# Kernel tuning notes

Hardware: AMD Instinct MI355X
Metric: run time of the kernel (lower is better)

## Reference

```python
import jax, jax.numpy as jnp
import numpy as np

N = 50000      # nodes
E = 800000     # edges (before self-loops)
D_IN = 64
D_OUT = 64


def setup_inputs() -> dict:
    key = jax.random.key(0)
    k1, k2, k3 = jax.random.split(key, 3)
    x = jax.random.normal(k1, (N, D_IN), dtype=jnp.float32)
    edge_index = jax.random.randint(k2, (2, E), 0, N, dtype=jnp.int64)
    # Glorot-ish init for the GCN linear weight
    W = jax.random.normal(k3, (D_IN, D_OUT), dtype=jnp.float32) * (1.0 / np.sqrt(D_IN))
    b = jnp.zeros((D_OUT,), dtype=jnp.float32)
    return {"x": x, "edge_index": edge_index, "W": W, "b": b}


def reference(x, edge_index, W, b):
    # GCNConv: add self-loops, symmetric normalization D^-1/2 (A+I) D^-1/2,
    # linear transform, scatter-add aggregation, bias; then ReLU.
    # Dropout is treated in eval mode (identity) for determinism.
    n = x.shape[0]
    loop = jnp.arange(n, dtype=edge_index.dtype)
    src = jnp.concatenate([edge_index[0], loop])  # [E+N]
    dst = jnp.concatenate([edge_index[1], loop])  # [E+N]

    ones = jnp.ones(src.shape[0], dtype=x.dtype)
    deg = jax.ops.segment_sum(ones, dst, num_segments=n)            # [N]
    dis = jnp.where(deg > 0, jax.lax.rsqrt(deg), 0.0)               # deg^-1/2
    norm = dis[src] * dis[dst]                                      # [E+N]

    xw = x @ W                                                      # [N, D_OUT]
    msgs = norm[:, None] * xw[src]                                  # [E+N, D_OUT]
    out = jax.ops.segment_sum(msgs, dst, num_segments=n) + b        # [N, D_OUT]
    return jax.nn.relu(out)
```

## Files before the change

### kernel.cpp

```cpp
#include <hip/hip_runtime.h>


#define TPB 256
#define STPB 512
#define MAXDEG 64
#define OVFCAP 8192
#define EPB 4096
#define MAXBIN 1024
#define MAXBLK 256

__device__ __forceinline__ int edges_are_i32(const unsigned* __restrict__ w) {
    int lane = threadIdx.x & 63;
    unsigned v = w[1 + 2 * lane];
    return __ballot(v != 0u) != 0ull;
}

__device__ __forceinline__ unsigned short f2bf(float f) {
    unsigned u = __float_as_uint(f);
    u += 0x7FFFu + ((u >> 16) & 1u);
    return (unsigned short)(u >> 16);
}
__device__ __forceinline__ float bf2f(unsigned short h) {
    return __uint_as_float(((unsigned)h) << 16);
}
__device__ __forceinline__ unsigned scale2(unsigned v, float dd) {
    unsigned lo = (unsigned)f2bf(dd * bf2f((unsigned short)(v & 0xFFFFu)));
    unsigned hi = (unsigned)f2bf(dd * bf2f((unsigned short)(v >> 16)));
    return lo | (hi << 16);
}

__device__ __forceinline__ void load4(const void* ei, int is32, long long base, int* v) {
    if (is32) {
        int4 a = *(const int4*)((const int*)ei + base);
        v[0] = a.x; v[1] = a.y; v[2] = a.z; v[3] = a.w;
    } else {
        longlong4 a = *(const longlong4*)((const long long*)ei + base);
        v[0] = (int)a.x; v[1] = (int)a.y; v[2] = (int)a.z; v[3] = (int)a.w;
    }
}

__global__ __launch_bounds__(256) void gemm_z0(const float* __restrict__ x,
                                               const float* __restrict__ W,
                                               unsigned short* __restrict__ z0,
                                               unsigned* __restrict__ ovf, int n) {
    if (blockIdx.x == 0 && threadIdx.x == 0) *ovf = 0u;

    __shared__ float lw[4096];
    const int t = threadIdx.x;
#pragma unroll
    for (int i = 0; i < 16; ++i) lw[i * 256 + t] = W[i * 256 + t];
    __syncthreads();

    const int lane = t & 63;
    const int wv   = t >> 6;
    const int row0 = blockIdx.x * 32 + wv * 8;
    if (row0 >= n) return;
    const int nr = (n - row0 >= 8) ? 8 : (n - row0);

    float acc[8] = {0.f, 0.f, 0.f, 0.f, 0.f, 0.f, 0.f, 0.f};
#pragma unroll
    for (int k0 = 0; k0 < 16; ++k0) {
        const float w0 = lw[(4 * k0 + 0) * 64 + lane];
        const float w1 = lw[(4 * k0 + 1) * 64 + lane];
        const float w2 = lw[(4 * k0 + 2) * 64 + lane];
        const float w3 = lw[(4 * k0 + 3) * 64 + lane];
#pragma unroll
        for (int r = 0; r < 8; ++r) {
            if (r < nr) {
                float4 xv = *(const float4*)(x + (long long)(row0 + r) * 64 + 4 * k0);
                acc[r] = fmaf(xv.w, w3, fmaf(xv.z, w2, fmaf(xv.y, w1,
                         fmaf(xv.x, w0, acc[r]))));
            }
        }
    }
#pragma unroll
    for (int r = 0; r < 8; ++r)
        if (r < nr) z0[(long long)(row0 + r) * 64 + lane] = f2bf(acc[r]);
}

__global__ __launch_bounds__(512) void binsort(const void* __restrict__ ei,
                                               unsigned* __restrict__ arena,
                                               uint2* __restrict__ desc,
                                               int E, int nbins, int nblocks) {
    __shared__ unsigned hist[MAXBIN];
    __shared__ unsigned bstart[MAXBIN];
    __shared__ unsigned cur[MAXBIN];
    __shared__ unsigned sorted[EPB];
    __shared__ unsigned partial[STPB];
    const int t   = threadIdx.x;
    const int blk = blockIdx.x;
    const long long base = (long long)blk * EPB;
    const int cnt = (int)((E - base < EPB) ? (E - base) : EPB);
    const int is32 = edges_are_i32((const unsigned*)ei);

    for (int i = t; i < nbins; i += STPB) hist[i] = 0u;
    __syncthreads();

    unsigned pay[8];
    unsigned short bn[8];
#pragma unroll
    for (int r = 0; r < 2; ++r) {
        const int lo = r * (STPB * 4) + t * 4;
        if (lo + 4 <= cnt) {
            int s4[4], d4[4];
            load4(ei, is32, base + lo, s4);
            load4(ei, is32, (long long)E + base + lo, d4);
#pragma unroll
            for (int k = 0; k < 4; ++k) {
                pay[r * 4 + k] = ((unsigned)(d4[k] & 63) << 16) | (unsigned)s4[k];
                bn[r * 4 + k]  = (unsigned short)((unsigned)d4[k] >> 6);
                atomicAdd(&hist[bn[r * 4 + k]], 1u);
            }
        } else {
#pragma unroll
            for (int k = 0; k < 4; ++k) {
                int l = lo + k;
                if (l < cnt) {
                    int s_, d_;
                    if (is32) {
                        s_ = ((const int*)ei)[base + l];
                        d_ = ((const int*)ei)[(long long)E + base + l];
                    } else {
                        s_ = (int)((const long long*)ei)[base + l];
                        d_ = (int)((const long long*)ei)[(long long)E + base + l];
                    }
                    pay[r * 4 + k] = ((unsigned)(d_ & 63) << 16) | (unsigned)s_;
                    bn[r * 4 + k]  = (unsigned short)((unsigned)d_ >> 6);
                    atomicAdd(&hist[bn[r * 4 + k]], 1u);
                } else {
                    bn[r * 4 + k] = 0xFFFFu;
                }
            }
        }
    }
    __syncthreads();

    unsigned s0 = 0;
#pragma unroll
    for (int k = 0; k < 2; ++k) { int bq = t * 2 + k; if (bq < nbins) s0 += hist[bq]; }
    partial[t] = s0;
    __syncthreads();
    for (int o = 1; o < STPB; o <<= 1) {
        unsigned v = (t >= o) ? partial[t - o] : 0u;
        __syncthreads();
        partial[t] += v;
        __syncthreads();
    }
    unsigned run = (t == 0) ? 0u : partial[t - 1];
#pragma unroll
    for (int k = 0; k < 2; ++k) {
        int bq = t * 2 + k;
        if (bq < nbins) { bstart[bq] = run; cur[bq] = run; run += hist[bq]; }
    }
    __syncthreads();

#pragma unroll
    for (int i = 0; i < 8; ++i) {
        if (bn[i] != 0xFFFFu) {
            unsigned p = atomicAdd(&cur[bn[i]], 1u);
            sorted[p] = pay[i];
        }
    }
    __syncthreads();

    for (int i = t; i < cnt; i += STPB) arena[base + i] = sorted[i];
    for (int bq = t; bq < nbins; bq += STPB) {
        uint2 dd;
        dd.x = (unsigned)(base + bstart[bq]);
        dd.y = hist[bq];
        desc[(long long)blk * nbins + bq] = dd;
    }
}

__global__ __launch_bounds__(256) void build_ell(const uint2* __restrict__ desc,
                                                 const unsigned* __restrict__ arena,
                                                 unsigned* __restrict__ fc,
                                                 unsigned short* __restrict__ ell,
                                                 unsigned* __restrict__ ovf,
                                                 int* __restrict__ ovfList,
                                                 unsigned short* __restrict__ z,
                                                 int n, int nbins, int nblocks) {
    __shared__ unsigned segstart[MAXBLK];
    __shared__ unsigned segpre[MAXBLK];
    __shared__ unsigned pre[256];
    __shared__ unsigned lcnt[MAXDEG];
    __shared__ __align__(16) unsigned short lell[MAXDEG * MAXDEG];
    const int t   = threadIdx.x;
    const int bin = blockIdx.x;
    const int base = bin * MAXDEG;

    if (t < MAXDEG) lcnt[t] = 0u;

    unsigned len = 0;
    if (t < nblocks) {
        uint2 dd = desc[(long long)t * nbins + bin];
        segstart[t] = dd.x;
        len = dd.y;
    }
    pre[t] = len;
    __syncthreads();
    for (int o = 1; o < 256; o <<= 1) {
        unsigned v = (t >= o) ? pre[t - o] : 0u;
        __syncthreads();
        pre[t] += v;
        __syncthreads();
    }
    const unsigned total = pre[255];
    if (t < nblocks) segpre[t] = pre[t] - len;
    __syncthreads();

    for (unsigned j = t; j < total; j += 256) {
        int lo = 0, hi = nblocks - 1;
        while (lo < hi) {
            int mid = (lo + hi + 1) >> 1;
            if (segpre[mid] <= j) lo = mid; else hi = mid - 1;
        }
        unsigned e  = arena[segstart[lo] + (j - segpre[lo])];
        unsigned dl = e >> 16;
        unsigned c  = atomicAdd(&lcnt[dl], 1u);
        if (c < MAXDEG) {
            lell[dl * MAXDEG + c] = (unsigned short)(e & 0xFFFFu);
        } else {
            unsigned p = atomicAdd(ovf, 1u);
            if (p < OVFCAP) {
                ovfList[2 * p]     = (int)(e & 0xFFFFu);
                ovfList[2 * p + 1] = base + (int)dl;
            }
        }
    }
    __syncthreads();

    const int maxrow = (n - base < MAXDEG) ? (n - base) : MAXDEG;
    if (t < maxrow) fc[base + t] = lcnt[t];

    const uint4* lp = (const uint4*)lell;
    uint4* gp = (uint4*)(ell + (long long)base * MAXDEG);
    for (int i = t; i < maxrow * 8; i += 256) gp[i] = lp[i];

    uint4* zp = (uint4*)(z + (long long)base * 64);
    for (int i = t; i < maxrow * 8; i += 256) {
        int row = i >> 3;
        float dd = rsqrtf(1.0f + (float)lcnt[row]);
        uint4 v = zp[i];
        v.x = scale2(v.x, dd); v.y = scale2(v.y, dd);
        v.z = scale2(v.z, dd); v.w = scale2(v.w, dd);
        zp[i] = v;
    }
}

__global__ __launch_bounds__(256) void gather_z(const unsigned short* __restrict__ ell,
                                                const unsigned* __restrict__ fc,
                                                const unsigned* __restrict__ ovf,
                                                const int* __restrict__ ovfList,
                                                const unsigned short* __restrict__ z,
                                                const float* __restrict__ b,
                                                float* __restrict__ out, int n) {
    const int wv   = (int)threadIdx.x >> 6;
    const int lane = threadIdx.x & 63;
    const int half = lane >> 5;
    const int cp   = lane & 31;
    const int node = (blockIdx.x * 4 + wv) * 2 + half;
    const bool valid = node < n;
    const int nodec = valid ? node : (n - 1);

    const unsigned deg = valid ? fc[nodec] : 0u;
    const float dd = rsqrtf(1.0f + (float)deg);

    unsigned zs = *(const unsigned*)(z + (unsigned)nodec * 64 + cp * 2);
    float acc0 = bf2f((unsigned short)(zs & 0xFFFFu));
    float acc1 = bf2f((unsigned short)(zs >> 16));

    unsigned m = deg < MAXDEG ? deg : MAXDEG;
    if (!valid) m = 0u;
    const unsigned mo = __shfl_xor((int)m, 32);
    const unsigned mmax = m > mo ? m : mo;

    const uint4* prow = (const uint4*)(ell + (unsigned)nodec * MAXDEG);

    unsigned i = 0;
    for (; i + 8 <= mmax; i += 8) {
        uint4 rw = prow[i >> 3];
        unsigned s[8];
        s[0] = rw.x & 0xFFFFu; s[1] = rw.x >> 16;
        s[2] = rw.y & 0xFFFFu; s[3] = rw.y >> 16;
        s[4] = rw.z & 0xFFFFu; s[5] = rw.z >> 16;
        s[6] = rw.w & 0xFFFFu; s[7] = rw.w >> 16;
        if (i + 8 <= m) {
            unsigned v[8];
#pragma unroll
            for (int k = 0; k < 8; ++k)
                v[k] = *(const unsigned*)(z + s[k] * 64u + cp * 2);
#pragma unroll
            for (int k = 0; k < 8; ++k) {
                acc0 += bf2f((unsigned short)(v[k] & 0xFFFFu));
                acc1 += bf2f((unsigned short)(v[k] >> 16));
            }
        } else {
#pragma unroll
            for (int k = 0; k < 8; ++k) {
                if (i + k < m) {
                    unsigned v = *(const unsigned*)(z + s[k] * 64u + cp * 2);
                    acc0 += bf2f((unsigned short)(v & 0xFFFFu));
                    acc1 += bf2f((unsigned short)(v >> 16));
                }
            }
        }
    }
    for (; i < mmax; ++i) {
        if (i < m) {
            unsigned s = ell[(unsigned)nodec * MAXDEG + i];
            unsigned v = *(const unsigned*)(z + s * 64u + cp * 2);
            acc0 += bf2f((unsigned short)(v & 0xFFFFu));
            acc1 += bf2f((unsigned short)(v >> 16));
        }
    }

    unsigned nov = *ovf;
    if (nov > 0) {
        nov = nov < OVFCAP ? nov : OVFCAP;
        for (unsigned j = 0; j < nov; ++j)
            if (valid && ovfList[2 * j + 1] == node) {
                unsigned v = *(const unsigned*)(z + (unsigned)ovfList[2 * j] * 64u + cp * 2);
                acc0 += bf2f((unsigned short)(v & 0xFFFFu));
                acc1 += bf2f((unsigned short)(v >> 16));
            }
    }

    if (valid) {
        float2 o;
        o.x = fmaxf(fmaf(dd, acc0, b[cp * 2 + 0]), 0.f);
        o.y = fmaxf(fmaf(dd, acc1, b[cp * 2 + 1]), 0.f);
        *(float2*)(out + (unsigned)node * 64 + cp * 2) = o;
    }
}

extern "C" void kernel_launch(void* const* d_in, const int* in_sizes, int n_in,
                              void* d_out, int out_size, void* d_ws, size_t ws_size,
                              hipStream_t stream) {
    const float* x  = (const float*)d_in[0];
    const void*  ei = d_in[1];
    const float* W  = (const float*)d_in[2];
    const float* b  = (const float*)d_in[3];
    float* out = (float*)d_out;

    const int n = in_sizes[0] / 64;
    const int E = in_sizes[1] / 2;
    const int nbins   = (n + MAXDEG - 1) / MAXDEG;
    const int nblocks = (E + EPB - 1) / EPB;

    unsigned short* z       = (unsigned short*)d_ws;
    unsigned short* ell     = z + (long long)n * 64;
    unsigned*       fc      = (unsigned*)(ell + (long long)n * 64);
    unsigned*       ovf     = fc + n;
    int*            ovfList = (int*)(ovf + 1);
    unsigned*       arena   = (unsigned*)(ovfList + 2 * OVFCAP);
    uint2*          desc    = (uint2*)(arena + E);

    gemm_z0<<<(n + 31) / 32, TPB, 0, stream>>>(x, W, z, ovf, n);
    binsort<<<nblocks, STPB, 0, stream>>>(ei, arena, desc, E, nbins, nblocks);
    build_ell<<<nbins, TPB, 0, stream>>>(desc, arena, fc, ell, ovf, ovfList, z,
                                         n, nbins, nblocks);
    gather_z<<<(n + 7) / 8, TPB, 0, stream>>>(ell, fc, ovf, ovfList, z, b, out, n);
}
```

Baseline: 83.12 us.

## Fuse GEMM and bin-sort into one launch and halve edges per sort block

The GEMM and bin-sort kernels are merged into one launch that splits work by block index, so the two independent stages run concurrently and one launch is saved. Edges per sort block drop from 4096 to 2048, which doubles the number of sort blocks, and build_ell's segment scan is widened to handle up to 512 segments. Shared memory is unioned between the two roles. In exchange, build_ell must scan and binary-search twice as many segments, and desc grows.

Result: faster. 80.92 us (-2.7%).

```diff
diff --git a/kernel.cpp b/kernel.cpp
--- a/kernel.cpp
+++ b/kernel.cpp
@@ -5,9 +5,9 @@
 #define STPB 512
 #define MAXDEG 64
 #define OVFCAP 8192
-#define EPB 4096
+#define EPB 2048
 #define MAXBIN 1024
-#define MAXBLK 256
+#define MAXBLK 512
 
 __device__ __forceinline__ int edges_are_i32(const unsigned* __restrict__ w) {
     int lane = threadIdx.x & 63;
@@ -39,56 +39,56 @@
     }
 }
 
-__global__ __launch_bounds__(256) void gemm_z0(const float* __restrict__ x,
-                                               const float* __restrict__ W,
-                                               unsigned short* __restrict__ z0,
-                                               unsigned* __restrict__ ovf, int n) {
-    if (blockIdx.x == 0 && threadIdx.x == 0) *ovf = 0u;
-
-    __shared__ float lw[4096];
+__global__ __launch_bounds__(512) void gemm_binsort(
+        const float* __restrict__ x, const float* __restrict__ W,
+        unsigned short* __restrict__ z0, unsigned* __restrict__ ovf,
+        const void* __restrict__ ei, unsigned* __restrict__ arena,
+        uint2* __restrict__ desc, int E, int nbins, int nblocks,
+        int n, int gemmBlocks) {
+    __shared__ __align__(16) unsigned char smem[22528];
     const int t = threadIdx.x;
-#pragma unroll
-    for (int i = 0; i < 16; ++i) lw[i * 256 + t] = W[i * 256 + t];
-    __syncthreads();
-
-    const int lane = t & 63;
-    const int wv   = t >> 6;
-    const int row0 = blockIdx.x * 32 + wv * 8;
-    if (row0 >= n) return;
-    const int nr = (n - row0 >= 8) ? 8 : (n - row0);
-
-    float acc[8] = {0.f, 0.f, 0.f, 0.f, 0.f, 0.f, 0.f, 0.f};
-#pragma unroll
-    for (int k0 = 0; k0 < 16; ++k0) {
-        const float w0 = lw[(4 * k0 + 0) * 64 + lane];
-        const float w1 = lw[(4 * k0 + 1) * 64 + lane];
-        const float w2 = lw[(4 * k0 + 2) * 64 + lane];
-        const float w3 = lw[(4 * k0 + 3) * 64 + lane];
-#pragma unroll
-        for (int r = 0; r < 8; ++r) {
-            if (r < nr) {
-                float4 xv = *(const float4*)(x + (long long)(row0 + r) * 64 + 4 * k0);
-                acc[r] = fmaf(xv.w, w3, fmaf(xv.z, w2, fmaf(xv.y, w1,
-                         fmaf(xv.x, w0, acc[r]))));
-            }
-        }
-    }
-#pragma unroll
-    for (int r = 0; r < 8; ++r)
-        if (r < nr) z0[(long long)(row0 + r) * 64 + lane] = f2bf(acc[r]);
-}
-
-__global__ __launch_bounds__(512) void binsort(const void* __restrict__ ei,
-                                               unsigned* __restrict__ arena,
-                                               uint2* __restrict__ desc,
-                                               int E, int nbins, int nblocks) {
-    __shared__ unsigned hist[MAXBIN];
-    __shared__ unsigned bstart[MAXBIN];
-    __shared__ unsigned cur[MAXBIN];
-    __shared__ unsigned sorted[EPB];
-    __shared__ unsigned partial[STPB];
-    const int t   = threadIdx.x;
-    const int blk = blockIdx.x;
+
+    if ((int)blockIdx.x < gemmBlocks) {
+        if (blockIdx.x == 0 && t == 0) *ovf = 0u;
+        float* lw = (float*)smem;
+#pragma unroll
+        for (int i = 0; i < 8; ++i) lw[i * 512 + t] = W[i * 512 + t];
+        __syncthreads();
+
+        const int lane = t & 63;
+        const int wv   = t >> 6;
+        const int row0 = blockIdx.x * 64 + wv * 8;
+        if (row0 >= n) return;
+        const int nr = (n - row0 >= 8) ? 8 : (n - row0);
+
+        float acc[8] = {0.f, 0.f, 0.f, 0.f, 0.f, 0.f, 0.f, 0.f};
+#pragma unroll
+        for (int k0 = 0; k0 < 16; ++k0) {
+            const float w0 = lw[(4 * k0 + 0) * 64 + lane];
+            const float w1 = lw[(4 * k0 + 1) * 64 + lane];
+            const float w2 = lw[(4 * k0 + 2) * 64 + lane];
+            const float w3 = lw[(4 * k0 + 3) * 64 + lane];
+#pragma unroll
+            for (int r = 0; r < 8; ++r) {
+                if (r < nr) {
+                    float4 xv = *(const float4*)(x + (long long)(row0 + r) * 64 + 4 * k0);
+                    acc[r] = fmaf(xv.w, w3, fmaf(xv.z, w2, fmaf(xv.y, w1,
+                             fmaf(xv.x, w0, acc[r]))));
+                }
+            }
+        }
+#pragma unroll
+        for (int r = 0; r < 8; ++r)
+            if (r < nr) z0[(long long)(row0 + r) * 64 + lane] = f2bf(acc[r]);
+        return;
+    }
+
+    unsigned* hist    = (unsigned*)smem;
+    unsigned* bstart  = hist + MAXBIN;
+    unsigned* cur     = bstart + MAXBIN;
+    unsigned* sorted  = cur + MAXBIN;
+    unsigned* partial = sorted + EPB;
+    const int blk = (int)blockIdx.x - gemmBlocks;
     const long long base = (long long)blk * EPB;
     const int cnt = (int)((E - base < EPB) ? (E - base) : EPB);
     const int is32 = edges_are_i32((const unsigned*)ei);
@@ -96,20 +96,19 @@
     for (int i = t; i < nbins; i += STPB) hist[i] = 0u;
     __syncthreads();
 
-    unsigned pay[8];
-    unsigned short bn[8];
-#pragma unroll
-    for (int r = 0; r < 2; ++r) {
-        const int lo = r * (STPB * 4) + t * 4;
+    unsigned pay[4];
+    unsigned short bn[4];
+    {
+        const int lo = t * 4;
         if (lo + 4 <= cnt) {
             int s4[4], d4[4];
             load4(ei, is32, base + lo, s4);
             load4(ei, is32, (long long)E + base + lo, d4);
 #pragma unroll
             for (int k = 0; k < 4; ++k) {
-                pay[r * 4 + k] = ((unsigned)(d4[k] & 63) << 16) | (unsigned)s4[k];
-                bn[r * 4 + k]  = (unsigned short)((unsigned)d4[k] >> 6);
-                atomicAdd(&hist[bn[r * 4 + k]], 1u);
+                pay[k] = ((unsigned)(d4[k] & 63) << 16) | (unsigned)s4[k];
+                bn[k]  = (unsigned short)((unsigned)d4[k] >> 6);
+                atomicAdd(&hist[bn[k]], 1u);
             }
         } else {
 #pragma unroll
@@ -124,11 +123,11 @@
                         s_ = (int)((const long long*)ei)[base + l];
                         d_ = (int)((const long long*)ei)[(long long)E + base + l];
                     }
-                    pay[r * 4 + k] = ((unsigned)(d_ & 63) << 16) | (unsigned)s_;
-                    bn[r * 4 + k]  = (unsigned short)((unsigned)d_ >> 6);
-                    atomicAdd(&hist[bn[r * 4 + k]], 1u);
+                    pay[k] = ((unsigned)(d_ & 63) << 16) | (unsigned)s_;
+                    bn[k]  = (unsigned short)((unsigned)d_ >> 6);
+                    atomicAdd(&hist[bn[k]], 1u);
                 } else {
-                    bn[r * 4 + k] = 0xFFFFu;
+                    bn[k] = 0xFFFFu;
                 }
             }
         }
@@ -155,7 +154,7 @@
     __syncthreads();
 
 #pragma unroll
-    for (int i = 0; i < 8; ++i) {
+    for (int i = 0; i < 4; ++i) {
         if (bn[i] != 0xFFFFu) {
             unsigned p = atomicAdd(&cur[bn[i]], 1u);
             sorted[p] = pay[i];
@@ -182,7 +181,7 @@
                                                  int n, int nbins, int nblocks) {
     __shared__ unsigned segstart[MAXBLK];
     __shared__ unsigned segpre[MAXBLK];
-    __shared__ unsigned pre[256];
+    __shared__ unsigned pre[MAXBLK];
     __shared__ unsigned lcnt[MAXDEG];
     __shared__ __align__(16) unsigned short lell[MAXDEG * MAXDEG];
     const int t   = threadIdx.x;
@@ -191,22 +190,34 @@
 
     if (t < MAXDEG) lcnt[t] = 0u;
 
-    unsigned len = 0;
+    unsigned len0 = 0, len1 = 0;
     if (t < nblocks) {
         uint2 dd = desc[(long long)t * nbins + bin];
         segstart[t] = dd.x;
-        len = dd.y;
-    }
-    pre[t] = len;
+        len0 = dd.y;
+    }
+    if (t + 256 < nblocks) {
+        uint2 dd = desc[(long long)(t + 256) * nbins + bin];
+        segstart[t + 256] = dd.x;
+        len1 = dd.y;
+    }
+    pre[t] = len0;
+    pre[t + 256] = len1;
     __syncthreads();
     for (int o = 1; o < 256; o <<= 1) {
-        unsigned v = (t >= o) ? pre[t - o] : 0u;
-        __syncthreads();
-        pre[t] += v;
-        __syncthreads();
-    }
-    const unsigned total = pre[255];
-    if (t < nblocks) segpre[t] = pre[t] - len;
+        unsigned vA = (t >= o) ? pre[t - o] : 0u;
+        unsigned vB = (t >= o) ? pre[256 + t - o] : 0u;
+        __syncthreads();
+        pre[t] += vA;
+        pre[256 + t] += vB;
+        __syncthreads();
+    }
+    const unsigned lowTot = pre[255];
+    pre[256 + t] += lowTot;
+    __syncthreads();
+    const unsigned total = pre[MAXBLK - 1];
+    if (t < nblocks) segpre[t] = pre[t] - len0;
+    if (t + 256 < nblocks) segpre[t + 256] = pre[256 + t] - len1;
     __syncthreads();
 
     for (unsigned j = t; j < total; j += 256) {
@@ -347,6 +358,7 @@
     const int E = in_sizes[1] / 2;
     const int nbins   = (n + MAXDEG - 1) / MAXDEG;
     const int nblocks = (E + EPB - 1) / EPB;
+    const int gemmBlocks = (n + 63) / 64;
 
     unsigned short* z       = (unsigned short*)d_ws;
     unsigned short* ell     = z + (long long)n * 64;
@@ -356,8 +368,8 @@
     unsigned*       arena   = (unsigned*)(ovfList + 2 * OVFCAP);
     uint2*          desc    = (uint2*)(arena + E);
 
-    gemm_z0<<<(n + 31) / 32, TPB, 0, stream>>>(x, W, z, ovf, n);
-    binsort<<<nblocks, STPB, 0, stream>>>(ei, arena, desc, E, nbins, nblocks);
+    gemm_binsort<<<gemmBlocks + nblocks, STPB, 0, stream>>>(
+        x, W, z, ovf, ei, arena, desc, E, nbins, nblocks, n, gemmBlocks);
     build_ell<<<nbins, TPB, 0, stream>>>(desc, arena, fc, ell, ovf, ovfList, z,
                                          n, nbins, nblocks);
     gather_z<<<(n + 7) / 8, TPB, 0, stream>>>(ell, fc, ovf, ovfList, z, b, out, n);
```
